# Kernel tuning notes

Hardware: AMD Instinct MI355X
Metric: run time of the kernel (lower is better)

The kernel has to match this reference:

```python
import jax, jax.numpy as jnp
import numpy as np

# ---- static config (mirrors init_kwargs) ----
B, A, NC = 16, 3, 80          # batch, anchors-per-head, classes
W = H = 76                     # grid (inputwidth / stride-8)
INPUTW = 608.0
M = 32                         # GT boxes per image
IGNORE = 0.5                   # ignore_thresh
MASK_N = 3                     # mask = [0,1,2] -> first 3 anchors belong to this head
ANCHORS = np.array([[10,13],[16,30],[33,23],[30,61],[62,45],[59,119],
                    [116,90],[156,198],[373,326]], dtype=np.float32)


def _box_iou(b1, b2):
    """b1 [N,4], b2 [P,4] xyxy -> iou [N,P] (same math as torch box_iou)."""
    area1 = (b1[:, 2] - b1[:, 0]) * (b1[:, 3] - b1[:, 1])
    area2 = (b2[:, 2] - b2[:, 0]) * (b2[:, 3] - b2[:, 1])
    lt = jnp.maximum(b1[:, None, :2], b2[None, :, :2])
    rb = jnp.minimum(b1[:, None, 2:], b2[None, :, 2:])
    inter = jnp.clip(rb - lt, 0.0).prod(-1)
    return inter / (area1[:, None] + area2[None, :] - inter)


def setup_inputs() -> dict:
    key = jax.random.key(0)
    k1, k2, k3, k4 = jax.random.split(key, 4)
    prediction = jax.random.normal(k1, (B, A * (5 + NC), W, H), jnp.float32) * 0.5
    # gt rows: (label, cx, cy, w, h, batch_idx), normalized coords, sorted by image
    labels = jax.random.randint(k2, (B * M, 1), 0, NC).astype(jnp.float32)
    cxy = jax.random.uniform(k3, (B * M, 2), minval=0.15, maxval=0.85)
    wh = jax.random.uniform(k4, (B * M, 2), minval=0.05, maxval=0.30)
    bidx = jnp.repeat(jnp.arange(B, dtype=jnp.float32), M)[:, None]
    gt = jnp.concatenate([labels, cxy, wh, bidx], axis=1)
    return {"prediction": prediction, "gt": gt}


def reference(prediction, gt):
    p = prediction.reshape(B, A, W, H, 5 + NC)
    cxp = jax.nn.sigmoid(p[..., 0])
    cyp = jax.nn.sigmoid(p[..., 1])
    wp, hp = p[..., 2], p[..., 3]
    confp = jax.nn.sigmoid(p[..., 4])
    classesp = jax.nn.sigmoid(p[..., 5:])
    # decode (anchors_g are the ORIGINAL pixel anchors: assigned before /strides)
    aw = jnp.asarray(ANCHORS[:MASK_N, 0]).reshape(1, A, 1, 1)
    ah = jnp.asarray(ANCHORS[:MASK_N, 1]).reshape(1, A, 1, 1)
    predx = cxp + jnp.arange(W, dtype=p.dtype)[None, None, None, :]
    predy = cyp + jnp.arange(H, dtype=p.dtype)[None, None, :, None]
    predw = jnp.exp(wp) * aw / INPUTW * W
    predh = jnp.exp(hp) * ah / INPUTW * H
    decoded = jnp.concatenate([predx[..., None], predy[..., None], predw[..., None],
                               predh[..., None], confp[..., None], classesp], axis=-1)

    # predicted boxes in pixel xyxy, flattened per image: [B, A*W*H, 4]
    x1 = (predx - predw * 0.5) / W * INPUTW
    y1 = (predy - predh * 0.5) / H * INPUTW
    x2 = (predx + predw * 0.5) / W * INPUTW
    y2 = (predy + predh * 0.5) / H * INPUTW
    pr = jnp.stack([x1, y1, x2, y2], axis=-1).reshape(B, -1, 4)

    # GT boxes per image (fixed M per image, rows sorted by batch idx)
    gtb = gt.reshape(B, M, 6)
    cx, cy, gw, gh = gtb[..., 1], gtb[..., 2], gtb[..., 3], gtb[..., 4]
    gxyxy = jnp.stack([(cx - gw * 0.5) * INPUTW, (cy - gh * 0.5) * INPUTW,
                       (cx + gw * 0.5) * INPUTW, (cy + gh * 0.5) * INPUTW], axis=-1)

    # per-image GT x all-preds IoU; noobj where best IoU <= ignore_thresh
    iou = jax.vmap(_box_iou)(gxyxy, pr)            # [B, M, A*W*H]
    maxv = iou.max(axis=1).reshape(B, A, H, W)      # W==H so flat order matches
    noobj = maxv <= IGNORE

    # best-anchor assignment per GT (vs all 9 anchors centered at the GT)
    ori = jnp.asarray(ANCHORS) / INPUTW             # [9,2] normalized
    fcx, fcy = cx.reshape(-1), cy.reshape(-1)       # [B*M]
    gflat = gxyxy.reshape(-1, 4)
    abox = jnp.stack([(fcx[:, None] - ori[None, :, 0] * 0.5) * INPUTW,
                      (fcy[:, None] - ori[None, :, 1] * 0.5) * INPUTW,
                      (fcx[:, None] + ori[None, :, 0] * 0.5) * INPUTW,
                      (fcy[:, None] + ori[None, :, 1] * 0.5) * INPUTW], axis=-1)  # [BM,9,4]
    lt = jnp.maximum(gflat[:, None, :2], abox[..., :2])
    rb = jnp.minimum(gflat[:, None, 2:], abox[..., 2:])
    inter = jnp.clip(rb - lt, 0.0).prod(-1)
    area_g = (gflat[:, 2] - gflat[:, 0]) * (gflat[:, 3] - gflat[:, 1])
    area_a = (abox[..., 2] - abox[..., 0]) * (abox[..., 3] - abox[..., 1])
    g_a = inter / (area_g[:, None] + area_a - inter)   # [BM,9]
    best = jnp.argmax(g_a, axis=1)
    valid = best < MASK_N                               # mask=[0,1,2] -> a_ind == best
    a_ind = jnp.clip(best, 0, MASK_N - 1)
    gi = (fcx * W).astype(jnp.int32)                    # original indexes dim-2 with x*width
    gj = (fcy * H).astype(jnp.int32)
    bb = jnp.repeat(jnp.arange(B), M)
    flat = ((bb * A + a_ind) * H + gi) * W + gj
    obj = jnp.zeros(B * A * H * W, bool).at[flat].max(valid).reshape(B, A, H, W)
    noobj = noobj.reshape(-1).at[flat].min(~valid).reshape(B, A, H, W)
    return decoded, noobj, obj
```

## Files before the change

### kernel.cpp

```cpp
#include <hip/hip_runtime.h>
#include <math.h>

#define BB 16
#define AA 3
#define NCC 80
#define WW 76
#define MM 32
#define CELLS_PER_IMG (AA * WW * WW)
#define NDECODE (BB * CELLS_PER_IMG * 85)
#define NCELLS (BB * CELLS_PER_IMG)
#define N4 (NDECODE / 4)

typedef float vfloat4 __attribute__((ext_vector_type(4)));

__constant__ float c_anchor[9][2] = {
    {10.f,13.f},{16.f,30.f},{33.f,23.f},{30.f,61.f},{62.f,45.f},
    {59.f,119.f},{116.f,90.f},{156.f,198.f},{373.f,326.f}};

#define LOG2E 1.4426950408889634f

__device__ __forceinline__ float fast_sigmoid(float x) {
    return __builtin_amdgcn_rcpf(1.0f + __builtin_amdgcn_exp2f(-x * LOG2E));
}

__device__ __forceinline__ vfloat4 sig4(vfloat4 v) {
    vfloat4 o;
    o.x = fast_sigmoid(v.x);
    o.y = fast_sigmoid(v.y);
    o.z = fast_sigmoid(v.z);
    o.w = fast_sigmoid(v.w);
    return o;
}

__device__ __forceinline__ void fix_chunk(unsigned i4, const vfloat4 v, vfloat4& o) {
    unsigned b = i4 * 4u;
    unsigned cell = (b + 3u) / 85u;
    int s = (int)(cell * 85u) - (int)b;
    if (s >= -3) {
        unsigned t  = cell / 76u;
        unsigned gi = cell - t * 76u;
        unsigned t2 = t / 76u;
        unsigned gj = t - t2 * 76u;
        unsigned a  = t2 % 3u;
        float aw = (a == 0u) ? 1.25f  : ((a == 1u) ? 2.0f  : 4.125f);
        float ah = (a == 0u) ? 1.625f : ((a == 1u) ? 3.75f : 2.875f);
        float q0 = (float)gi, q1 = (float)gj;
        float raw[4] = {v.x, v.y, v.z, v.w};
        float sg[4]  = {o.x, o.y, o.z, o.w};
        float res[4] = {o.x, o.y, o.z, o.w};
#pragma unroll
        for (int j = 0; j < 4; ++j) {
            int k = j - s;
            if ((unsigned)k < 4u) {
                float e    = __builtin_amdgcn_exp2f(raw[j] * LOG2E);
                float addq = (k == 0) ? q0 : q1;
                float an   = (k == 2) ? aw : ah;
                float val  = (k < 2) ? (sg[j] + addq) : (e * an);
                res[j] = val;
            }
        }
        o.x = res[0]; o.y = res[1]; o.z = res[2]; o.w = res[3];
    }
}

__global__ __launch_bounds__(256) void decode_kernel(const vfloat4* __restrict__ in,
                                                     vfloat4* __restrict__ out,
                                                     const float* __restrict__ pred,
                                                     float4* __restrict__ boxes) {
    unsigned tid  = blockIdx.x * 256u + threadIdx.x;
    unsigned wave = tid >> 6;
    unsigned lane = tid & 63u;
    unsigned i0 = wave * 256u + lane;
    unsigned i1 = i0 + 64u;
    unsigned i2 = i0 + 128u;
    unsigned i3 = i0 + 192u;
    const unsigned last = N4 - 1u;

    vfloat4 v0 = in[i0 < last ? i0 : last];
    vfloat4 v1 = in[i1 < last ? i1 : last];
    vfloat4 v2 = in[i2 < last ? i2 : last];
    vfloat4 v3 = in[i3 < last ? i3 : last];

    bool p0 = i0 < N4, p1 = i1 < N4, p2 = i2 < N4, p3 = i3 < N4;

    vfloat4 o0 = sig4(v0);
    vfloat4 o1 = sig4(v1);
    vfloat4 o2 = sig4(v2);
    vfloat4 o3 = sig4(v3);

    if (p0) fix_chunk(i0, v0, o0);
    if (p1) fix_chunk(i1, v1, o1);
    if (p2) fix_chunk(i2, v2, o2);
    if (p3) fix_chunk(i3, v3, o3);

    if (p0) __builtin_nontemporal_store(o0, &out[i0]);
    if (p1) __builtin_nontemporal_store(o1, &out[i1]);
    if (p2) __builtin_nontemporal_store(o2, &out[i2]);
    if (p3) __builtin_nontemporal_store(o3, &out[i3]);

    unsigned span = wave * 1024u;
    unsigned c0 = (span + 84u) / 85u;
    unsigned c  = c0 + lane;
    unsigned ws = c * 85u;
    if (lane < 13u && ws < span + 1024u && c < (unsigned)NCELLS) {
        const float* p = pred + ws;
        float t0 = p[0], t1 = p[1], t2v = p[2], t3v = p[3];
        unsigned tq  = c / 76u;
        unsigned gi  = c - tq * 76u;
        unsigned tq2 = tq / 76u;
        unsigned gj  = tq - tq2 * 76u;
        unsigned a   = tq2 % 3u;
        float aw = (a == 0u) ? 1.25f  : ((a == 1u) ? 2.0f  : 4.125f);
        float ah = (a == 0u) ? 1.625f : ((a == 1u) ? 3.75f : 2.875f);
        float px = fast_sigmoid(t0) + (float)gi;
        float py = fast_sigmoid(t1) + (float)gj;
        float pw = __builtin_amdgcn_exp2f(t2v * LOG2E) * aw;
        float ph = __builtin_amdgcn_exp2f(t3v * LOG2E) * ah;
        boxes[c] = make_float4(px, py, pw, ph);
    }
}

__global__ void noobj_kernel(const float4* __restrict__ boxes, const float* __restrict__ gt,
                             float* __restrict__ noobj, float* __restrict__ obj) {
    __shared__ float4 sbox[MM];
    int b = blockIdx.y;
    int t = threadIdx.x;
    if (t < MM) {
        const float* g = gt + (size_t)(b * MM + t) * 6;
        float cx = g[1], cy = g[2], gw = g[3], gh = g[4];
        sbox[t] = make_float4((cx - gw * 0.5f) * 608.0f, (cy - gh * 0.5f) * 608.0f,
                              (cx + gw * 0.5f) * 608.0f, (cy + gh * 0.5f) * 608.0f);
    }
    __syncthreads();
    int n = blockIdx.x * blockDim.x + t;
    if (n >= CELLS_PER_IMG) return;
    size_t idx = (size_t)b * CELLS_PER_IMG + n;
    float4 pb = boxes[idx];
    float px = pb.x, py = pb.y, pw = pb.z, ph = pb.w;
    float x1 = (px - pw * 0.5f) / 76.0f * 608.0f;
    float y1 = (py - ph * 0.5f) / 76.0f * 608.0f;
    float x2 = (px + pw * 0.5f) / 76.0f * 608.0f;
    float y2 = (py + ph * 0.5f) / 76.0f * 608.0f;
    float area2 = (x2 - x1) * (y2 - y1);
    float best = 0.0f;
#pragma unroll
    for (int m = 0; m < MM; ++m) {
        float4 gb = sbox[m];
        float area1 = (gb.z - gb.x) * (gb.w - gb.y);
        float ltx = fmaxf(gb.x, x1), lty = fmaxf(gb.y, y1);
        float rbx = fminf(gb.z, x2), rby = fminf(gb.w, y2);
        float inter = fmaxf(rbx - ltx, 0.0f) * fmaxf(rby - lty, 0.0f);
        float iou = inter * __builtin_amdgcn_rcpf(area1 + area2 - inter);
        best = fmaxf(best, iou);
    }
    noobj[idx] = (best <= 0.5f) ? 1.0f : 0.0f;
    obj[idx] = 0.0f;
}

__global__ void assign_kernel(const float* __restrict__ gt,
                              float* __restrict__ noobj, float* __restrict__ obj) {
    int r = blockIdx.x * blockDim.x + threadIdx.x;
    if (r >= BB * MM) return;
    const float* g = gt + (size_t)r * 6;
    float cx = g[1], cy = g[2], gw = g[3], gh = g[4];
    float gx1 = (cx - gw * 0.5f) * 608.0f, gy1 = (cy - gh * 0.5f) * 608.0f;
    float gx2 = (cx + gw * 0.5f) * 608.0f, gy2 = (cy + gh * 0.5f) * 608.0f;
    float area_g = (gx2 - gx1) * (gy2 - gy1);
    int best = 0;
    float bestv = -1.0f;
#pragma unroll
    for (int k = 0; k < 9; ++k) {
        float ow = c_anchor[k][0] / 608.0f, oh = c_anchor[k][1] / 608.0f;
        float ax1 = (cx - ow * 0.5f) * 608.0f, ay1 = (cy - oh * 0.5f) * 608.0f;
        float ax2 = (cx + ow * 0.5f) * 608.0f, ay2 = (cy + oh * 0.5f) * 608.0f;
        float ltx = fmaxf(gx1, ax1), lty = fmaxf(gy1, ay1);
        float rbx = fminf(gx2, ax2), rby = fminf(gy2, ay2);
        float inter = fmaxf(rbx - ltx, 0.0f) * fmaxf(rby - lty, 0.0f);
        float area_a = (ax2 - ax1) * (ay2 - ay1);
        float v = inter / (area_g + area_a - inter);
        if (v > bestv) { bestv = v; best = k; }
    }
    if (best < AA) {
        int b = r / MM;
        int gi = (int)(cx * 76.0f);
        int gj = (int)(cy * 76.0f);
        int flat = ((b * AA + best) * WW + gi) * WW + gj;
        obj[flat] = 1.0f;
        noobj[flat] = 0.0f;
    }
}

extern "C" void kernel_launch(void* const* d_in, const int* in_sizes, int n_in,
                              void* d_out, int out_size, void* d_ws, size_t ws_size,
                              hipStream_t stream) {
    const float* pred = (const float*)d_in[0];
    const float* gt   = (const float*)d_in[1];
    float* dec   = (float*)d_out;
    float* noobj = dec + NDECODE;
    float* obj   = noobj + NCELLS;
    float4* boxes = (float4*)d_ws;

    const int nblocks = (N4 + 1023) / 1024;
    decode_kernel<<<nblocks, 256, 0, stream>>>(
        (const vfloat4*)pred, (vfloat4*)dec, pred, boxes);

    dim3 gb((CELLS_PER_IMG + 255) / 256, BB);
    noobj_kernel<<<gb, 256, 0, stream>>>(boxes, gt, noobj, obj);

    assign_kernel<<<2, 256, 0, stream>>>(gt, noobj, obj);
}
```

Baseline: 192.4 us.

## Fuse noobj IoU computation into decode kernel, dropping boxes buffer

The per-cell IoU-versus-GT max and the noobj/obj writes move into the decode kernel, which now stages up to two images' GT boxes in shared memory per block. This removes one kernel launch and the round trip through the intermediate boxes buffer in workspace. In exchange only 13 lanes per wave do the 32-box IoU loop, which adds serialized ALU work to the memory-bound decode kernel, and every block now pays a barrier.

```diff
diff --git a/kernel.cpp b/kernel.cpp
--- a/kernel.cpp
+++ b/kernel.cpp
@@ -66,7 +66,27 @@
 __global__ __launch_bounds__(256) void decode_kernel(const vfloat4* __restrict__ in,
                                                      vfloat4* __restrict__ out,
                                                      const float* __restrict__ pred,
-                                                     float4* __restrict__ boxes) {
+                                                     const float* __restrict__ gt,
+                                                     float* __restrict__ noobj,
+                                                     float* __restrict__ obj) {
+    __shared__ float4 sbox[2 * MM];
+    unsigned span_blk = blockIdx.x * 4096u;
+    unsigned cblk0    = (span_blk + 84u) / 85u;
+    unsigned bi0      = cblk0 / (unsigned)CELLS_PER_IMG;
+    if (threadIdx.x < 64u) {
+        unsigned m  = threadIdx.x & 31u;
+        unsigned bi = bi0 + (threadIdx.x >> 5);
+        if (bi < (unsigned)BB) {
+            const float* g = gt + (size_t)(bi * MM + m) * 6;
+            float cx = g[1], cy = g[2], gw = g[3], gh = g[4];
+            sbox[threadIdx.x] = make_float4((cx - gw * 0.5f) * 608.0f,
+                                            (cy - gh * 0.5f) * 608.0f,
+                                            (cx + gw * 0.5f) * 608.0f,
+                                            (cy + gh * 0.5f) * 608.0f);
+        }
+    }
+    __syncthreads();
+
     unsigned tid  = blockIdx.x * 256u + threadIdx.x;
     unsigned wave = tid >> 6;
     unsigned lane = tid & 63u;
@@ -101,9 +121,9 @@
     unsigned span = wave * 1024u;
     unsigned c0 = (span + 84u) / 85u;
     unsigned c  = c0 + lane;
-    unsigned ws = c * 85u;
-    if (lane < 13u && ws < span + 1024u && c < (unsigned)NCELLS) {
-        const float* p = pred + ws;
+    unsigned wstart = c * 85u;
+    if (lane < 13u && wstart < span + 1024u && c < (unsigned)NCELLS) {
+        const float* p = pred + wstart;
         float t0 = p[0], t1 = p[1], t2v = p[2], t3v = p[3];
         unsigned tq  = c / 76u;
         unsigned gi  = c - tq * 76u;
@@ -116,45 +136,27 @@
         float py = fast_sigmoid(t1) + (float)gj;
         float pw = __builtin_amdgcn_exp2f(t2v * LOG2E) * aw;
         float ph = __builtin_amdgcn_exp2f(t3v * LOG2E) * ah;
-        boxes[c] = make_float4(px, py, pw, ph);
-    }
-}
-
-__global__ void noobj_kernel(const float4* __restrict__ boxes, const float* __restrict__ gt,
-                             float* __restrict__ noobj, float* __restrict__ obj) {
-    __shared__ float4 sbox[MM];
-    int b = blockIdx.y;
-    int t = threadIdx.x;
-    if (t < MM) {
-        const float* g = gt + (size_t)(b * MM + t) * 6;
-        float cx = g[1], cy = g[2], gw = g[3], gh = g[4];
-        sbox[t] = make_float4((cx - gw * 0.5f) * 608.0f, (cy - gh * 0.5f) * 608.0f,
-                              (cx + gw * 0.5f) * 608.0f, (cy + gh * 0.5f) * 608.0f);
-    }
-    __syncthreads();
-    int n = blockIdx.x * blockDim.x + t;
-    if (n >= CELLS_PER_IMG) return;
-    size_t idx = (size_t)b * CELLS_PER_IMG + n;
-    float4 pb = boxes[idx];
-    float px = pb.x, py = pb.y, pw = pb.z, ph = pb.w;
-    float x1 = (px - pw * 0.5f) / 76.0f * 608.0f;
-    float y1 = (py - ph * 0.5f) / 76.0f * 608.0f;
-    float x2 = (px + pw * 0.5f) / 76.0f * 608.0f;
-    float y2 = (py + ph * 0.5f) / 76.0f * 608.0f;
-    float area2 = (x2 - x1) * (y2 - y1);
-    float best = 0.0f;
+
+        float x1 = (px - pw * 0.5f) / 76.0f * 608.0f;
+        float y1 = (py - ph * 0.5f) / 76.0f * 608.0f;
+        float x2 = (px + pw * 0.5f) / 76.0f * 608.0f;
+        float y2 = (py + ph * 0.5f) / 76.0f * 608.0f;
+        float area2 = (x2 - x1) * (y2 - y1);
+        unsigned li = (c / (unsigned)CELLS_PER_IMG - bi0) * 32u;
+        float best = 0.0f;
 #pragma unroll
-    for (int m = 0; m < MM; ++m) {
-        float4 gb = sbox[m];
-        float area1 = (gb.z - gb.x) * (gb.w - gb.y);
-        float ltx = fmaxf(gb.x, x1), lty = fmaxf(gb.y, y1);
-        float rbx = fminf(gb.z, x2), rby = fminf(gb.w, y2);
-        float inter = fmaxf(rbx - ltx, 0.0f) * fmaxf(rby - lty, 0.0f);
-        float iou = inter * __builtin_amdgcn_rcpf(area1 + area2 - inter);
-        best = fmaxf(best, iou);
-    }
-    noobj[idx] = (best <= 0.5f) ? 1.0f : 0.0f;
-    obj[idx] = 0.0f;
+        for (int m = 0; m < MM; ++m) {
+            float4 gb = sbox[li + m];
+            float area1 = (gb.z - gb.x) * (gb.w - gb.y);
+            float ltx = fmaxf(gb.x, x1), lty = fmaxf(gb.y, y1);
+            float rbx = fminf(gb.z, x2), rby = fminf(gb.w, y2);
+            float inter = fmaxf(rbx - ltx, 0.0f) * fmaxf(rby - lty, 0.0f);
+            float iou = inter * __builtin_amdgcn_rcpf(area1 + area2 - inter);
+            best = fmaxf(best, iou);
+        }
+        noobj[c] = (best <= 0.5f) ? 1.0f : 0.0f;
+        obj[c] = 0.0f;
+    }
 }
 
 __global__ void assign_kernel(const float* __restrict__ gt,
@@ -198,14 +200,11 @@
     float* dec   = (float*)d_out;
     float* noobj = dec + NDECODE;
     float* obj   = noobj + NCELLS;
-    float4* boxes = (float4*)d_ws;
+    (void)d_ws; (void)ws_size;
 
     const int nblocks = (N4 + 1023) / 1024;
     decode_kernel<<<nblocks, 256, 0, stream>>>(
-        (const vfloat4*)pred, (vfloat4*)dec, pred, boxes);
-
-    dim3 gb((CELLS_PER_IMG + 255) / 256, BB);
-    noobj_kernel<<<gb, 256, 0, stream>>>(boxes, gt, noobj, obj);
+        (const vfloat4*)pred, (vfloat4*)dec, pred, gt, noobj, obj);
 
     assign_kernel<<<2, 256, 0, stream>>>(gt, noobj, obj);
 }
```

Result: faster. 179.8 us (-6.6%).
